# Optimization experiments

Measured on AMD Instinct MI355X. Metric: run time of the kernel, lower is better.

## Reference

```python
import jax, jax.numpy as jnp
import numpy as np

# Constants from the torch module __init__
FACE_INDS = np.array([[0, 1, 2, 3], [0, 4, 2, 6], [0, 1, 4, 5],
                      [1, 3, 5, 7], [2, 3, 6, 7], [4, 5, 6, 7]])  # (6,4)
N_GRID = 11
N_POINTS = N_GRID * N_GRID        # 121
N_FACE = 6
N_KP_HAND = 21
N_CONTACTS = 10
ITA = 0.2
IND1 = np.array([0, 1, 2, 3])
IND2 = np.array([1, 2, 3, 0])


def _bilinear_grid():
    # grid[p, k] = bilinear weights for the 4 face corners, p over 11x11 (u,v)
    g = []
    for u in np.linspace(0.0, 1.0, N_GRID):
        for v in np.linspace(0.0, 1.0, N_GRID):
            g.append([v * (1 - u), v * u, (1 - v) * (1 - u), u * (1 - v)])
    return jnp.asarray(np.array(g, dtype=np.float32))  # (121, 4)


def setup_inputs() -> dict:
    key = jax.random.key(0)
    poses = jax.random.normal(key, (8192, N_KP_HAND + 8, 3), dtype=jnp.float32)
    return {"poses": poses}


def affinity_loss(poses):
    bs = poses.shape[0]
    hand = poses[:, :N_KP_HAND, :]          # (bs, 21, 3)
    obj = poses[:, N_KP_HAND:, :]           # (bs, 8, 3)

    # --- sample_face_points: bilinear sample 121 pts on each of the 6 faces ---
    grid = _bilinear_grid().astype(poses.dtype)        # (121, 4)
    faces = obj[:, FACE_INDS, :]                        # (bs, 6, 4, 3)
    face_points = jnp.einsum('bfkc,pk->bfpc', faces, grid)  # (bs, 6, 121, 3)
    obj_pts = face_points.reshape(bs, N_FACE * N_POINTS, 3)  # (bs, 726, 3)

    xx = jnp.sum(hand * hand, axis=-1)                  # (bs, 21)
    yy = jnp.sum(obj_pts * obj_pts, axis=-1)            # (bs, 726)
    zz = jnp.einsum('bic,bjc->bij', hand, obj_pts)      # (bs, 21, 726)
    pdist = jnp.sqrt(xx[:, :, None] + yy[:, None, :] - 2.0 * zz + 1e-6)
    pdist = pdist.reshape(bs, N_KP_HAND, N_FACE, N_POINTS)

    # --- per (hand kp, face) nearest face point, then global top-10 contacts ---
    dist_h2f = jnp.min(pdist, axis=3)                   # (bs, 21, 6)
    idxs_h2f = jnp.argmin(pdist, axis=3)                # (bs, 21, 6)
    flat = dist_h2f.reshape(bs, N_KP_HAND * N_FACE)     # (bs, 126)
    order = jnp.argsort(flat, axis=1)[:, :N_CONTACTS]   # (bs, 10)
    dist = jnp.take_along_axis(flat, order, axis=1)     # (bs, 10)
    inds_hand = order // N_FACE
    inds_face = order % N_FACE
    b = jnp.arange(bs)[:, None]
    ind_obj = idxs_h2f[b, inds_hand, inds_face]                     # (bs, 10)
    obj_contacts = obj_pts[b, inds_face * N_POINTS + ind_obj]       # (bs, 10, 3)

    # --- get_obj_info: axis endpoints and mean edge length of the bbox ---
    points1 = obj[:, :4, :].mean(axis=1)                # (bs, 3)
    points2 = obj[:, 4:, :].mean(axis=1)                # (bs, 3)
    l1 = jnp.linalg.norm(obj[:, IND1] - obj[:, IND2], axis=-1).mean(1, keepdims=True)
    l2 = jnp.linalg.norm(obj[:, IND1 + 4] - obj[:, IND2 + 4], axis=-1).mean(1, keepdims=True)
    length = (l1 + l2) * 0.5                            # (bs, 1)

    mask1 = (dist < length * ITA).astype(poses.dtype)   # (bs, 10)
    mask = mask1[:, :, None] * mask1[:, None, :]        # (bs, 10, 10)

    direct_vec = points2 - points1                      # (bs, 3)
    dv_norm = jnp.linalg.norm(direct_vec, axis=1, keepdims=True)  # (bs, 1)
    normed_dv = direct_vec / (dv_norm + 1e-5)
    vec_contacts = obj_contacts - points1[:, None, :]   # (bs, 10, 3)
    inner = jnp.sum(direct_vec[:, None, :] * vec_contacts, axis=-1)  # (bs, 10)
    t = inner / (dv_norm + 1e-5)                        # (bs, 10)
    r = points1[:, None, :] + normed_dv[:, None, :] * t[:, :, None]  # (bs, 10, 3)
    normal_vec = obj_contacts - r
    normal_vec = normal_vec / (jnp.linalg.norm(normal_vec, axis=2, keepdims=True) + 1e-5)
    cos_sim = jnp.einsum('bic,bjc->bij', normal_vec, normal_vec)  # (bs, 10, 10)

    return (cos_sim * mask).sum() / (mask.sum() + 1.0)


def reference(poses):
    return affinity_loss(poses)
```

## Files before the change

kernel.cpp:

```cpp
#include <hip/hip_runtime.h>
#include <math.h>

#define NGRID   11
#define NPAIR   126
#define NCONT   10

#define NSUB    64
#define NBUK    128
#define WS_SUB  16
#define WS_BUK  128
#define WS_WORDS (WS_BUK + 2 * NBUK)

#define NBUCKET 256

typedef float v2f __attribute__((ext_vector_type(2)));
#define FMA2(a,b,c) __builtin_elementwise_fma((a),(b),(c))
#define MAX2(a,b)   __builtin_elementwise_max((a),(b))
#define SP2(x)      ((v2f){(x),(x)})

__device__ __constant__ int4 c_face4[6] = {
    {0,1,2,3},{0,4,2,6},{0,1,4,5},{1,3,5,7},{2,3,6,7},{4,5,6,7}};
__device__ __constant__ float c_U[NGRID] = {
    0.0f,0.1f,0.2f,0.3f,0.4f,0.5f,0.6f,0.7f,0.8f,0.9f,1.0f};

__global__ void zero_ws_kernel(float* ws, int n) {
    int t = blockIdx.x * 256 + threadIdx.x;
    if (t < n) ws[t] = 0.0f;
}

__device__ __forceinline__ void pair_coefs(
        const float* __restrict__ obj, float hx, float hy, float hz, int f,
        float& C00, float& C10, float& C01, float& C11,
        float& C20, float& C02, float& C21, float& C12, float& C22) {
    const int4 F = c_face4[f];
    float av[3], bv[3], cv[3], dv[3];
    #pragma unroll
    for (int c = 0; c < 3; ++c) {
        const float P0 = obj[F.x * 3 + c];
        const float P1 = obj[F.y * 3 + c];
        const float P2 = obj[F.z * 3 + c];
        const float P3 = obj[F.w * 3 + c];
        av[c] = P2;
        bv[c] = P3 - P2;
        cv[c] = P0 - P2;
        dv[c] = P1 - P0 - P3 + P2;
    }
    float aa=0.f,bb=0.f,cc=0.f,dd=0.f,ab=0.f,ac=0.f,ad=0.f,bc=0.f,bd=0.f,cd=0.f;
    #pragma unroll
    for (int c = 0; c < 3; ++c) {
        aa += av[c]*av[c]; bb += bv[c]*bv[c];
        cc += cv[c]*cv[c]; dd += dv[c]*dv[c];
        ab += av[c]*bv[c]; ac += av[c]*cv[c];
        ad += av[c]*dv[c]; bc += bv[c]*cv[c];
        bd += bv[c]*dv[c]; cd += cv[c]*dv[c];
    }
    const float hx2 = 2.0f*hx, hy2 = 2.0f*hy, hz2 = 2.0f*hz;
    const float ha2 = fmaf(hx2, av[0], fmaf(hy2, av[1], hz2*av[2]));
    const float hb2 = fmaf(hx2, bv[0], fmaf(hy2, bv[1], hz2*bv[2]));
    const float hc2 = fmaf(hx2, cv[0], fmaf(hy2, cv[1], hz2*cv[2]));
    const float hd2 = fmaf(hx2, dv[0], fmaf(hy2, dv[1], hz2*dv[2]));
    C00 = ha2 - aa;
    C10 = hb2 - 2.f*ab;
    C01 = hc2 - 2.f*ac;
    C11 = hd2 - 2.f*(ad + bc);
    C20 = -bb;  C02 = -cc;  C21 = -2.f*bd;  C12 = -2.f*cd;  C22 = -dd;
}

__device__ __forceinline__ void scan_pair(
        const float* __restrict__ obj, const float* __restrict__ hand,
        int pair, float& d2s, int& ru_out) {
    const int i = pair / 6;
    const int f = pair - i * 6;
    const float hx = hand[i*3+0], hy = hand[i*3+1], hz = hand[i*3+2];
    const float xx = hx*hx + hy*hy + hz*hz;
    float C00,C10,C01,C11,C20,C02,C21,C12,C22;
    pair_coefs(obj, hx, hy, hz, f, C00,C10,C01,C11,C20,C02,C21,C12,C22);

    const float U[NGRID] = {0.0f,0.1f,0.2f,0.3f,0.4f,0.5f,
                            0.6f,0.7f,0.8f,0.9f,1.0f};
    float qb = -3.0e38f;
    int   ru = 0;
    #pragma unroll
    for (int rp = 0; rp < 5; ++rp) {
        const v2f u2 = (v2f){U[2*rp], U[2*rp+1]};
        const v2f A2 = FMA2(FMA2(SP2(C22), u2, SP2(C12)), u2, SP2(C02));
        const v2f A1 = FMA2(FMA2(SP2(C21), u2, SP2(C11)), u2, SP2(C01));
        const v2f A0 = FMA2(FMA2(SP2(C20), u2, SP2(C10)), u2, SP2(C00));
        v2f m2 = A0;
        #pragma unroll
        for (int iv = 1; iv < NGRID; ++iv) {
            const v2f vv = SP2(U[iv]);
            m2 = MAX2(m2, FMA2(FMA2(A2, vv, A1), vv, A0));
        }
        if (m2.x > qb) { qb = m2.x; ru = 2*rp; }
        if (m2.y > qb) { qb = m2.y; ru = 2*rp + 1; }
    }
    {
        const float A2 = fmaf(fmaf(C22,1.f,C12),1.f,C02);
        const float A1 = fmaf(fmaf(C21,1.f,C11),1.f,C01);
        const float A0 = fmaf(fmaf(C20,1.f,C10),1.f,C00);
        float m1 = A0;
        #pragma unroll
        for (int iv = 1; iv < NGRID; ++iv)
            m1 = fmaxf(m1, fmaf(fmaf(A2,U[iv],A1),U[iv],A0));
        if (m1 > qb) { qb = m1; ru = 10; }
    }
    d2s = xx - qb;
    ru_out = ru;
}

__launch_bounds__(256)
__global__ void affinity_kernel(const float* __restrict__ poses,
                                float* __restrict__ ws,
                                float* __restrict__ out,
                                int bs, int nw, int mode) {
    const int lane = threadIdx.x & 63;
    const int wv   = threadIdx.x >> 6;
    const int gw   = blockIdx.x * 4 + wv;
    const bool valid = gw < bs;

    __shared__ float    sh_pose[4][88];
    __shared__ unsigned sh_cand[4][128];
    __shared__ unsigned sh_keys[4][128];
    float*    pose = sh_pose[wv];
    unsigned* cand = sh_cand[wv];
    unsigned* keys = sh_keys[wv];

    if (valid) {
        const float* src = poses + (size_t)gw * 87;
        pose[lane] = src[lane];
        if (lane < 23) pose[64 + lane] = src[64 + lane];
    }
    __threadfence_block();

    float num = 0.f, dnm = 0.f;
    if (valid) {
        const float* hand = pose;
        const float* obj  = pose + 63;

        float l1 = 0.0f, l2 = 0.0f;
        #pragma unroll
        for (int e = 0; e < 4; ++e) {
            const int a = e, b2 = (e + 1) & 3;
            {
                const float dx = obj[a*3+0]-obj[b2*3+0];
                const float dy = obj[a*3+1]-obj[b2*3+1];
                const float dz = obj[a*3+2]-obj[b2*3+2];
                l1 += sqrtf(dx*dx + dy*dy + dz*dz);
            }
            {
                const float dx = obj[(a+4)*3+0]-obj[(b2+4)*3+0];
                const float dy = obj[(a+4)*3+1]-obj[(b2+4)*3+1];
                const float dz = obj[(a+4)*3+2]-obj[(b2+4)*3+2];
                l2 += sqrtf(dx*dx + dy*dy + dz*dz);
            }
        }
        l1 *= 0.25f; l2 *= 0.25f;
        const float L02  = (l1 + l2) * 0.5f * 0.2f;
        const float thrF = L02 * L02 - 1e-6f + 1e-2f;

        float d2A; int ruA;
        scan_pair(obj, hand, lane, d2A, ruA);
        const bool flagA = d2A < thrF;
        const bool hasB  = (lane + 64) < NPAIR;
        float d2B = 3.0e38f; int ruB = 0;
        if (hasB) scan_pair(obj, hand, lane + 64, d2B, ruB);
        const bool flagB = hasB && (d2B < thrF);

        const unsigned long long lt = (1ull << lane) - 1ull;
        const unsigned long long mA = __ballot(flagA);
        const unsigned long long mB = __ballot(flagB);
        const int cntA = __popcll(mA);
        const int cnt  = cntA + __popcll(mB);
        if (flagA) cand[__popcll(mA & lt)] =
            (unsigned)lane | ((unsigned)ruA << 8);
        if (flagB) cand[cntA + __popcll(mB & lt)] =
            (unsigned)(lane + 64) | ((unsigned)ruB << 8);
        __threadfence_block();

        float rkey[2]; float rcx[2], rcy[2], rcz[2]; int rval[2] = {0, 0};
        int n2 = 0;
        #pragma unroll
        for (int c = 0; c < 2; ++c) {
            if (c == 1 && cnt <= 64) break;
            const int idx = c * 64 + lane;
            const bool act = idx < cnt;
            bool pass = false; unsigned key = 0;
            float cx = 0.f, cy = 0.f, cz = 0.f;
            if (act) {
                const unsigned rec = cand[idx];
                const int pair = rec & 0xFF;
                const int ru   = rec >> 8;
                const int i = pair / 6;
                const int f = pair - 6 * i;
                const float hx = hand[i*3+0], hy = hand[i*3+1], hz = hand[i*3+2];
                float C00,C10,C01,C11,C20,C02,C21,C12,C22;
                pair_coefs(obj, hx, hy, hz, f,
                           C00,C10,C01,C11,C20,C02,C21,C12,C22);
                const float u  = c_U[ru];
                const float A2 = fmaf(fmaf(C22,u,C12),u,C02);
                const float A1 = fmaf(fmaf(C21,u,C11),u,C01);
                const float A0 = fmaf(fmaf(C20,u,C10),u,C00);
                const float U[NGRID] = {0.0f,0.1f,0.2f,0.3f,0.4f,0.5f,
                                        0.6f,0.7f,0.8f,0.9f,1.0f};
                float qr = A0; int vb = 0;
                #pragma unroll
                for (int iv = 1; iv < NGRID; ++iv) {
                    const float q = fmaf(fmaf(A2,U[iv],A1),U[iv],A0);
                    if (q > qr) { qr = q; vb = iv; }
                }
                const double du = ru * 0.1;
                const double dv = vb * 0.1;
                const float w0 = (float)(dv * (1.0 - du));
                const float w1 = (float)(dv * du);
                const float w2 = (float)((1.0 - dv) * (1.0 - du));
                const float w3 = (float)(du * (1.0 - dv));
                const int4 F = c_face4[f];
                const int i0 = F.x*3, i1 = F.y*3, i2 = F.z*3, i3 = F.w*3;
                cx = w0*obj[i0+0]+w1*obj[i1+0]+w2*obj[i2+0]+w3*obj[i3+0];
                cy = w0*obj[i0+1]+w1*obj[i1+1]+w2*obj[i2+1]+w3*obj[i3+1];
                cz = w0*obj[i0+2]+w1*obj[i1+2]+w2*obj[i2+2]+w3*obj[i3+2];
                const float xx = hx*hx + hy*hy + hz*hz;
                const float yy = cx*cx + cy*cy + cz*cz;
                const float zz = hx*cx + hy*cy + hz*cz;
                const float d2e = (xx + yy) - 2.0f * zz;
                const float dist = sqrtf(d2e + 1e-6f);
                pass = dist < L02;
                key = (__float_as_uint(fmaxf(d2e, 0.0f)) & 0xFFFFFF80u)
                    | (unsigned)pair;
            }
            const unsigned long long mp = __ballot(pass);
            if (pass) {
                keys[n2 + __popcll(mp & lt)] = key;
                rkey[c] = __uint_as_float(key);
                rcx[c] = cx; rcy[c] = cy; rcz[c] = cz;
                rval[c] = 1;
            }
            n2 += __popcll(mp);
        }
        __threadfence_block();

        const int kwin = n2 < NCONT ? n2 : NCONT;
        float px = 0.f, py = 0.f, pz = 0.f;
        if (rval[0] | rval[1]) {
            const float p1x = (((obj[0] +obj[3]) +obj[6]) +obj[9]) *0.25f;
            const float p1y = (((obj[1] +obj[4]) +obj[7]) +obj[10])*0.25f;
            const float p1z = (((obj[2] +obj[5]) +obj[8]) +obj[11])*0.25f;
            const float p2x = (((obj[12]+obj[15])+obj[18])+obj[21])*0.25f;
            const float p2y = (((obj[13]+obj[16])+obj[19])+obj[22])*0.25f;
            const float p2z = (((obj[14]+obj[17])+obj[20])+obj[23])*0.25f;
            const float dvx = p2x-p1x, dvy = p2y-p1y, dvz = p2z-p1z;
            const float dvn = sqrtf(dvx*dvx + dvy*dvy + dvz*dvz);
            const float den = dvn + 1e-5f;
            const float ndx = dvx/den, ndy = dvy/den, ndz = dvz/den;
            #pragma unroll
            for (int c = 0; c < 2; ++c) {
                if (!rval[c]) continue;
                const unsigned myk = __float_as_uint(rkey[c]);
                int rank = 0;
                for (int j = 0; j < n2; ++j) rank += (keys[j] < myk) ? 1 : 0;
                if (rank < NCONT) {
                    const float cx = rcx[c], cy = rcy[c], cz = rcz[c];
                    const float vcx = cx-p1x, vcy = cy-p1y, vcz = cz-p1z;
                    const float inner = dvx*vcx + dvy*vcy + dvz*vcz;
                    const float tp = inner / den;
                    const float rx = p1x + ndx*tp, ry = p1y + ndy*tp,
                                rz = p1z + ndz*tp;
                    const float nvx = cx-rx, nvy = cy-ry, nvz = cz-rz;
                    const float nvn = sqrtf(nvx*nvx + nvy*nvy + nvz*nvz)
                                    + 1e-5f;
                    px += nvx / nvn; py += nvy / nvn; pz += nvz / nvn;
                }
            }
        }
        #pragma unroll
        for (int off = 32; off >= 1; off >>= 1) {
            px += __shfl_xor(px, off, 64);
            py += __shfl_xor(py, off, 64);
            pz += __shfl_xor(pz, off, 64);
        }
        if (lane == 0) {
            num = px*px + py*py + pz*pz;
            dnm = (float)(kwin * kwin);
        }
    }

    int last = 0;
    if (lane == 0) {
        if (mode) {
            float* bkt = ws + WS_BUK + 2 * (gw & (NBUK - 1));
            const float r0 = atomicAdd(bkt + 0, num);
            const float r1 = atomicAdd(bkt + 1, dnm);
            asm volatile("" :: "v"(r0), "v"(r1) : "memory");
            unsigned* subs = (unsigned*)ws + WS_SUB;
            const unsigned g = (unsigned)gw & (NSUB - 1);
            const unsigned quota = ((unsigned)nw - 1u - g) / NSUB + 1u;
            const unsigned old = atomicAdd(subs + g, 1u);
            if (old + 1u == quota) {
                const unsigned ngroups =
                    (unsigned)nw < NSUB ? (unsigned)nw : NSUB;
                const unsigned m2 = atomicAdd((unsigned*)ws, 1u);
                if (m2 + 1u == ngroups) last = 1;
            }
        } else {
            float* bucket = ws + 2 * (gw & (NBUCKET - 1));
            atomicAdd(bucket + 0, num);
            atomicAdd(bucket + 1, dnm);
        }
    }
    last = __shfl(last, 0, 64);

    if (last) {
        double n = 0.0, d = 0.0;
        for (int k = lane; k < NBUK; k += 64) {
            float* bkt = ws + WS_BUK + 2 * k;
            n += (double)atomicAdd(bkt + 0, 0.0f);
            d += (double)atomicAdd(bkt + 1, 0.0f);
        }
        #pragma unroll
        for (int off = 32; off >= 1; off >>= 1) {
            n += __shfl_xor(n, off, 64);
            d += __shfl_xor(d, off, 64);
        }
        if (lane == 0) out[0] = (float)(n / (d + 1.0));
    }
}

__launch_bounds__(1024)
__global__ void finalize_kernel(const float* __restrict__ ws,
                                float* __restrict__ out, int nslot) {
    const int t = threadIdx.x;
    __shared__ double sh_n[16], sh_d[16];
    double n = 0.0, d = 0.0;
    for (int k = t; k < nslot; k += 1024) {
        n += (double)ws[2 * k + 0];
        d += (double)ws[2 * k + 1];
    }
    #pragma unroll
    for (int off = 32; off >= 1; off >>= 1) {
        n += __shfl_xor(n, off, 64);
        d += __shfl_xor(d, off, 64);
    }
    const int w = t >> 6;
    if ((t & 63) == 0) { sh_n[w] = n; sh_d[w] = d; }
    __syncthreads();
    if (t == 0) {
        double nn = 0.0, dd = 0.0;
        #pragma unroll
        for (int i = 0; i < 16; ++i) { nn += sh_n[i]; dd += sh_d[i]; }
        out[0] = (float)(nn / (dd + 1.0));
    }
}

extern "C" void kernel_launch(void* const* d_in, const int* in_sizes, int n_in,
                              void* d_out, int out_size, void* d_ws, size_t ws_size,
                              hipStream_t stream) {
    const float* poses = (const float*)d_in[0];
    float* out = (float*)d_out;
    float* ws  = (float*)d_ws;
    const int bs = in_sizes[0] / 87;
    const int nblk = (bs + 3) / 4;
    const int nw   = nblk * 4;

    if (ws_size >= (size_t)WS_WORDS * sizeof(float)) {
        hipMemsetAsync(ws, 0, WS_WORDS * sizeof(float), stream);
        hipLaunchKernelGGL(affinity_kernel, dim3(nblk), dim3(256), 0, stream,
                           poses, ws, out, bs, nw, 1);
    } else {
        hipLaunchKernelGGL(zero_ws_kernel, dim3(1), dim3(256), 0, stream,
                           ws, NBUCKET * 2);
        hipLaunchKernelGGL(affinity_kernel, dim3(nblk), dim3(256), 0, stream,
                           poses, ws, out, bs, nw, 0);
        hipLaunchKernelGGL(finalize_kernel, dim3(1), dim3(1024), 0, stream,
                           ws, out, NBUCKET);
    }
}
```

Measured before the change: 90.16 us.

## Split pair scan into separate full-occupancy kernel feeding a select kernel

```diff
diff --git a/kernel.cpp b/kernel.cpp
--- a/kernel.cpp
+++ b/kernel.cpp
@@ -9,7 +9,8 @@
 #define NBUK    128
 #define WS_SUB  16
 #define WS_BUK  128
-#define WS_WORDS (WS_BUK + 2 * NBUK)
+#define WS_HDR  384
+#define WS_REC  1024
 
 #define NBUCKET 256
 
@@ -109,11 +110,95 @@
     ru_out = ru;
 }
 
+__device__ __forceinline__ void exact_contact(
+        const float* __restrict__ obj, const float* __restrict__ hand,
+        int pair, int ru, float& cx, float& cy, float& cz, float& d2e) {
+    const int i = pair / 6;
+    const int f = pair - 6 * i;
+    const float hx = hand[i*3+0], hy = hand[i*3+1], hz = hand[i*3+2];
+    float C00,C10,C01,C11,C20,C02,C21,C12,C22;
+    pair_coefs(obj, hx, hy, hz, f, C00,C10,C01,C11,C20,C02,C21,C12,C22);
+    const float u  = c_U[ru];
+    const float A2 = fmaf(fmaf(C22,u,C12),u,C02);
+    const float A1 = fmaf(fmaf(C21,u,C11),u,C01);
+    const float A0 = fmaf(fmaf(C20,u,C10),u,C00);
+    const float U[NGRID] = {0.0f,0.1f,0.2f,0.3f,0.4f,0.5f,
+                            0.6f,0.7f,0.8f,0.9f,1.0f};
+    float qr = A0; int vb = 0;
+    #pragma unroll
+    for (int iv = 1; iv < NGRID; ++iv) {
+        const float q = fmaf(fmaf(A2,U[iv],A1),U[iv],A0);
+        if (q > qr) { qr = q; vb = iv; }
+    }
+    const double du = ru * 0.1;
+    const double dv = vb * 0.1;
+    const float w0 = (float)(dv * (1.0 - du));
+    const float w1 = (float)(dv * du);
+    const float w2 = (float)((1.0 - dv) * (1.0 - du));
+    const float w3 = (float)(du * (1.0 - dv));
+    const int4 F = c_face4[f];
+    const int i0 = F.x*3, i1 = F.y*3, i2 = F.z*3, i3 = F.w*3;
+    cx = w0*obj[i0+0]+w1*obj[i1+0]+w2*obj[i2+0]+w3*obj[i3+0];
+    cy = w0*obj[i0+1]+w1*obj[i1+1]+w2*obj[i2+1]+w3*obj[i3+1];
+    cz = w0*obj[i0+2]+w1*obj[i1+2]+w2*obj[i2+2]+w3*obj[i3+2];
+    const float xx = hx*hx + hy*hy + hz*hz;
+    const float yy = cx*cx + cy*cy + cz*cz;
+    const float zz = hx*cx + hy*cy + hz*cz;
+    d2e = (xx + yy) - 2.0f * zz;
+}
+
+__device__ __forceinline__ float length_thr(const float* __restrict__ obj) {
+    float l1 = 0.0f, l2 = 0.0f;
+    #pragma unroll
+    for (int e = 0; e < 4; ++e) {
+        const int a = e, b2 = (e + 1) & 3;
+        {
+            const float dx = obj[a*3+0]-obj[b2*3+0];
+            const float dy = obj[a*3+1]-obj[b2*3+1];
+            const float dz = obj[a*3+2]-obj[b2*3+2];
+            l1 += sqrtf(dx*dx + dy*dy + dz*dz);
+        }
+        {
+            const float dx = obj[(a+4)*3+0]-obj[(b2+4)*3+0];
+            const float dy = obj[(a+4)*3+1]-obj[(b2+4)*3+1];
+            const float dz = obj[(a+4)*3+2]-obj[(b2+4)*3+2];
+            l2 += sqrtf(dx*dx + dy*dy + dz*dz);
+        }
+    }
+    l1 *= 0.25f; l2 *= 0.25f;
+    return (l1 + l2) * 0.5f * 0.2f;
+}
+
 __launch_bounds__(256)
-__global__ void affinity_kernel(const float* __restrict__ poses,
-                                float* __restrict__ ws,
-                                float* __restrict__ out,
-                                int bs, int nw, int mode) {
+__global__ void scan_kernel(const float* __restrict__ poses,
+                            float* __restrict__ ws, int bs) {
+    const int t = threadIdx.x;
+    const int half = t >> 7;
+    const int t0 = t & 127;
+    const int batch = blockIdx.x * 2 + half;
+    __shared__ float sh_pose[2][88];
+
+    if (blockIdx.x == 0) {
+        for (int w = t; w < WS_HDR; w += 256) ws[w] = 0.0f;
+    }
+    const bool valid = batch < bs;
+    if (valid && t0 < 87) sh_pose[half][t0] = poses[(size_t)batch * 87 + t0];
+    __syncthreads();
+    if (!valid) return;
+    unsigned rec = __float_as_uint(3.0e38f) & 0xFFFFFFF0u;
+    if (t0 < NPAIR) {
+        float d2s; int ru;
+        scan_pair(sh_pose[half] + 63, sh_pose[half], t0, d2s, ru);
+        rec = (__float_as_uint(d2s) & 0xFFFFFFF0u) | (unsigned)ru;
+    }
+    ((unsigned*)ws)[WS_REC + (size_t)batch * 128 + t0] = rec;
+}
+
+__launch_bounds__(256)
+__global__ void select_kernel(const float* __restrict__ poses,
+                              float* __restrict__ ws,
+                              float* __restrict__ out,
+                              int bs, int nw) {
     const int lane = threadIdx.x & 63;
     const int wv   = threadIdx.x >> 6;
     const int gw   = blockIdx.x * 4 + wv;
@@ -126,46 +211,23 @@
     unsigned* cand = sh_cand[wv];
     unsigned* keys = sh_keys[wv];
 
+    float num = 0.f, dnm = 0.f;
     if (valid) {
         const float* src = poses + (size_t)gw * 87;
         pose[lane] = src[lane];
         if (lane < 23) pose[64 + lane] = src[64 + lane];
-    }
-    __threadfence_block();
-
-    float num = 0.f, dnm = 0.f;
-    if (valid) {
+        const unsigned* recs = (const unsigned*)ws + WS_REC + (size_t)gw * 128;
+        const unsigned recA = recs[lane];
+        const unsigned recB = recs[lane + 64];
+        __threadfence_block();
+
         const float* hand = pose;
         const float* obj  = pose + 63;
-
-        float l1 = 0.0f, l2 = 0.0f;
-        #pragma unroll
-        for (int e = 0; e < 4; ++e) {
-            const int a = e, b2 = (e + 1) & 3;
-            {
-                const float dx = obj[a*3+0]-obj[b2*3+0];
-                const float dy = obj[a*3+1]-obj[b2*3+1];
-                const float dz = obj[a*3+2]-obj[b2*3+2];
-                l1 += sqrtf(dx*dx + dy*dy + dz*dz);
-            }
-            {
-                const float dx = obj[(a+4)*3+0]-obj[(b2+4)*3+0];
-                const float dy = obj[(a+4)*3+1]-obj[(b2+4)*3+1];
-                const float dz = obj[(a+4)*3+2]-obj[(b2+4)*3+2];
-                l2 += sqrtf(dx*dx + dy*dy + dz*dz);
-            }
-        }
-        l1 *= 0.25f; l2 *= 0.25f;
-        const float L02  = (l1 + l2) * 0.5f * 0.2f;
+        const float L02  = length_thr(obj);
         const float thrF = L02 * L02 - 1e-6f + 1e-2f;
 
-        float d2A; int ruA;
-        scan_pair(obj, hand, lane, d2A, ruA);
-        const bool flagA = d2A < thrF;
-        const bool hasB  = (lane + 64) < NPAIR;
-        float d2B = 3.0e38f; int ruB = 0;
-        if (hasB) scan_pair(obj, hand, lane + 64, d2B, ruB);
-        const bool flagB = hasB && (d2B < thrF);
+        const bool flagA = __uint_as_float(recA & 0xFFFFFFF0u) < thrF;
+        const bool flagB = __uint_as_float(recB & 0xFFFFFFF0u) < thrF;
 
         const unsigned long long lt = (1ull << lane) - 1ull;
         const unsigned long long mA = __ballot(flagA);
@@ -173,9 +235,9 @@
         const int cntA = __popcll(mA);
         const int cnt  = cntA + __popcll(mB);
         if (flagA) cand[__popcll(mA & lt)] =
-            (unsigned)lane | ((unsigned)ruA << 8);
+            (unsigned)lane | ((recA & 0xFu) << 8);
         if (flagB) cand[cntA + __popcll(mB & lt)] =
-            (unsigned)(lane + 64) | ((unsigned)ruB << 8);
+            (unsigned)(lane + 64) | ((recB & 0xFu) << 8);
         __threadfence_block();
 
         float rkey[2]; float rcx[2], rcy[2], rcz[2]; int rval[2] = {0, 0};
@@ -188,42 +250,11 @@
             bool pass = false; unsigned key = 0;
             float cx = 0.f, cy = 0.f, cz = 0.f;
             if (act) {
-                const unsigned rec = cand[idx];
-                const int pair = rec & 0xFF;
-                const int ru   = rec >> 8;
-                const int i = pair / 6;
-                const int f = pair - 6 * i;
-                const float hx = hand[i*3+0], hy = hand[i*3+1], hz = hand[i*3+2];
-                float C00,C10,C01,C11,C20,C02,C21,C12,C22;
-                pair_coefs(obj, hx, hy, hz, f,
-                           C00,C10,C01,C11,C20,C02,C21,C12,C22);
-                const float u  = c_U[ru];
-                const float A2 = fmaf(fmaf(C22,u,C12),u,C02);
-                const float A1 = fmaf(fmaf(C21,u,C11),u,C01);
-                const float A0 = fmaf(fmaf(C20,u,C10),u,C00);
-                const float U[NGRID] = {0.0f,0.1f,0.2f,0.3f,0.4f,0.5f,
-                                        0.6f,0.7f,0.8f,0.9f,1.0f};
-                float qr = A0; int vb = 0;
-                #pragma unroll
-                for (int iv = 1; iv < NGRID; ++iv) {
-                    const float q = fmaf(fmaf(A2,U[iv],A1),U[iv],A0);
-                    if (q > qr) { qr = q; vb = iv; }
-                }
-                const double du = ru * 0.1;
-                const double dv = vb * 0.1;
-                const float w0 = (float)(dv * (1.0 - du));
-                const float w1 = (float)(dv * du);
-                const float w2 = (float)((1.0 - dv) * (1.0 - du));
-                const float w3 = (float)(du * (1.0 - dv));
-                const int4 F = c_face4[f];
-                const int i0 = F.x*3, i1 = F.y*3, i2 = F.z*3, i3 = F.w*3;
-                cx = w0*obj[i0+0]+w1*obj[i1+0]+w2*obj[i2+0]+w3*obj[i3+0];
-                cy = w0*obj[i0+1]+w1*obj[i1+1]+w2*obj[i2+1]+w3*obj[i3+1];
-                cz = w0*obj[i0+2]+w1*obj[i1+2]+w2*obj[i2+2]+w3*obj[i3+2];
-                const float xx = hx*hx + hy*hy + hz*hz;
-                const float yy = cx*cx + cy*cy + cz*cz;
-                const float zz = hx*cx + hy*cy + hz*cz;
-                const float d2e = (xx + yy) - 2.0f * zz;
+                const unsigned rc = cand[idx];
+                const int pair = rc & 0xFF;
+                const int ru   = rc >> 8;
+                float d2e;
+                exact_contact(obj, hand, pair, ru, cx, cy, cz, d2e);
                 const float dist = sqrtf(d2e + 1e-6f);
                 pass = dist < L02;
                 key = (__float_as_uint(fmaxf(d2e, 0.0f)) & 0xFFFFFF80u)
@@ -287,25 +318,19 @@
 
     int last = 0;
     if (lane == 0) {
-        if (mode) {
-            float* bkt = ws + WS_BUK + 2 * (gw & (NBUK - 1));
-            const float r0 = atomicAdd(bkt + 0, num);
-            const float r1 = atomicAdd(bkt + 1, dnm);
-            asm volatile("" :: "v"(r0), "v"(r1) : "memory");
-            unsigned* subs = (unsigned*)ws + WS_SUB;
-            const unsigned g = (unsigned)gw & (NSUB - 1);
-            const unsigned quota = ((unsigned)nw - 1u - g) / NSUB + 1u;
-            const unsigned old = atomicAdd(subs + g, 1u);
-            if (old + 1u == quota) {
-                const unsigned ngroups =
-                    (unsigned)nw < NSUB ? (unsigned)nw : NSUB;
-                const unsigned m2 = atomicAdd((unsigned*)ws, 1u);
-                if (m2 + 1u == ngroups) last = 1;
-            }
-        } else {
-            float* bucket = ws + 2 * (gw & (NBUCKET - 1));
-            atomicAdd(bucket + 0, num);
-            atomicAdd(bucket + 1, dnm);
+        float* bkt = ws + WS_BUK + 2 * (gw & (NBUK - 1));
+        const float r0 = atomicAdd(bkt + 0, num);
+        const float r1 = atomicAdd(bkt + 1, dnm);
+        asm volatile("" :: "v"(r0), "v"(r1) : "memory");
+        unsigned* subs = (unsigned*)ws + WS_SUB;
+        const unsigned g = (unsigned)gw & (NSUB - 1);
+        const unsigned quota = ((unsigned)nw - 1u - g) / NSUB + 1u;
+        const unsigned old = atomicAdd(subs + g, 1u);
+        if (old + 1u == quota) {
+            const unsigned ngroups =
+                (unsigned)nw < NSUB ? (unsigned)nw : NSUB;
+            const unsigned m2 = atomicAdd((unsigned*)ws, 1u);
+            if (m2 + 1u == ngroups) last = 1;
         }
     }
     last = __shfl(last, 0, 64);
@@ -323,6 +348,136 @@
             d += __shfl_xor(d, off, 64);
         }
         if (lane == 0) out[0] = (float)(n / (d + 1.0));
+    }
+}
+
+__launch_bounds__(256)
+__global__ void affinity_fallback(const float* __restrict__ poses,
+                                  float* __restrict__ ws, int bs) {
+    const int lane = threadIdx.x & 63;
+    const int wv   = threadIdx.x >> 6;
+    const int gw   = blockIdx.x * 4 + wv;
+    const bool valid = gw < bs;
+
+    __shared__ float    sh_pose[4][88];
+    __shared__ unsigned sh_cand[4][128];
+    __shared__ unsigned sh_keys[4][128];
+    float*    pose = sh_pose[wv];
+    unsigned* cand = sh_cand[wv];
+    unsigned* keys = sh_keys[wv];
+
+    if (valid) {
+        const float* src = poses + (size_t)gw * 87;
+        pose[lane] = src[lane];
+        if (lane < 23) pose[64 + lane] = src[64 + lane];
+    }
+    __threadfence_block();
+
+    float num = 0.f, dnm = 0.f;
+    if (valid) {
+        const float* hand = pose;
+        const float* obj  = pose + 63;
+        const float L02  = length_thr(obj);
+        const float thrF = L02 * L02 - 1e-6f + 1e-2f;
+
+        float d2A; int ruA;
+        scan_pair(obj, hand, lane, d2A, ruA);
+        const bool flagA = d2A < thrF;
+        const bool hasB  = (lane + 64) < NPAIR;
+        float d2B = 3.0e38f; int ruB = 0;
+        if (hasB) scan_pair(obj, hand, lane + 64, d2B, ruB);
+        const bool flagB = hasB && (d2B < thrF);
+
+        const unsigned long long lt = (1ull << lane) - 1ull;
+        const unsigned long long mA = __ballot(flagA);
+        const unsigned long long mB = __ballot(flagB);
+        const int cntA = __popcll(mA);
+        const int cnt  = cntA + __popcll(mB);
+        if (flagA) cand[__popcll(mA & lt)] =
+            (unsigned)lane | ((unsigned)ruA << 8);
+        if (flagB) cand[cntA + __popcll(mB & lt)] =
+            (unsigned)(lane + 64) | ((unsigned)ruB << 8);
+        __threadfence_block();
+
+        float rkey[2]; float rcx[2], rcy[2], rcz[2]; int rval[2] = {0, 0};
+        int n2 = 0;
+        #pragma unroll
+        for (int c = 0; c < 2; ++c) {
+            if (c == 1 && cnt <= 64) break;
+            const int idx = c * 64 + lane;
+            const bool act = idx < cnt;
+            bool pass = false; unsigned key = 0;
+            float cx = 0.f, cy = 0.f, cz = 0.f;
+            if (act) {
+                const unsigned rc = cand[idx];
+                const int pair = rc & 0xFF;
+                const int ru   = rc >> 8;
+                float d2e;
+                exact_contact(obj, hand, pair, ru, cx, cy, cz, d2e);
+                const float dist = sqrtf(d2e + 1e-6f);
+                pass = dist < L02;
+                key = (__float_as_uint(fmaxf(d2e, 0.0f)) & 0xFFFFFF80u)
+                    | (unsigned)pair;
+            }
+            const unsigned long long mp = __ballot(pass);
+            if (pass) {
+                keys[n2 + __popcll(mp & lt)] = key;
+                rkey[c] = __uint_as_float(key);
+                rcx[c] = cx; rcy[c] = cy; rcz[c] = cz;
+                rval[c] = 1;
+            }
+            n2 += __popcll(mp);
+        }
+        __threadfence_block();
+
+        const int kwin = n2 < NCONT ? n2 : NCONT;
+        float px = 0.f, py = 0.f, pz = 0.f;
+        if (rval[0] | rval[1]) {
+            const float p1x = (((obj[0] +obj[3]) +obj[6]) +obj[9]) *0.25f;
+            const float p1y = (((obj[1] +obj[4]) +obj[7]) +obj[10])*0.25f;
+            const float p1z = (((obj[2] +obj[5]) +obj[8]) +obj[11])*0.25f;
+            const float p2x = (((obj[12]+obj[15])+obj[18])+obj[21])*0.25f;
+            const float p2y = (((obj[13]+obj[16])+obj[19])+obj[22])*0.25f;
+            const float p2z = (((obj[14]+obj[17])+obj[20])+obj[23])*0.25f;
+            const float dvx = p2x-p1x, dvy = p2y-p1y, dvz = p2z-p1z;
+            const float dvn = sqrtf(dvx*dvx + dvy*dvy + dvz*dvz);
+            const float den = dvn + 1e-5f;
+            const float ndx = dvx/den, ndy = dvy/den, ndz = dvz/den;
+            #pragma unroll
+            for (int c = 0; c < 2; ++c) {
+                if (!rval[c]) continue;
+                const unsigned myk = __float_as_uint(rkey[c]);
+                int rank = 0;
+                for (int j = 0; j < n2; ++j) rank += (keys[j] < myk) ? 1 : 0;
+                if (rank < NCONT) {
+                    const float cx = rcx[c], cy = rcy[c], cz = rcz[c];
+                    const float vcx = cx-p1x, vcy = cy-p1y, vcz = cz-p1z;
+                    const float inner = dvx*vcx + dvy*vcy + dvz*vcz;
+                    const float tp = inner / den;
+                    const float rx = p1x + ndx*tp, ry = p1y + ndy*tp,
+                                rz = p1z + ndz*tp;
+                    const float nvx = cx-rx, nvy = cy-ry, nvz = cz-rz;
+                    const float nvn = sqrtf(nvx*nvx + nvy*nvy + nvz*nvz)
+                                    + 1e-5f;
+                    px += nvx / nvn; py += nvy / nvn; pz += nvz / nvn;
+                }
+            }
+        }
+        #pragma unroll
+        for (int off = 32; off >= 1; off >>= 1) {
+            px += __shfl_xor(px, off, 64);
+            py += __shfl_xor(py, off, 64);
+            pz += __shfl_xor(pz, off, 64);
+        }
+        if (lane == 0) {
+            num = px*px + py*py + pz*pz;
+            dnm = (float)(kwin * kwin);
+        }
+    }
+    if (lane == 0) {
+        float* bucket = ws + 2 * (gw & (NBUCKET - 1));
+        atomicAdd(bucket + 0, num);
+        atomicAdd(bucket + 1, dnm);
     }
 }
 
@@ -359,18 +514,22 @@
     float* out = (float*)d_out;
     float* ws  = (float*)d_ws;
     const int bs = in_sizes[0] / 87;
-    const int nblk = (bs + 3) / 4;
-    const int nw   = nblk * 4;
-
-    if (ws_size >= (size_t)WS_WORDS * sizeof(float)) {
-        hipMemsetAsync(ws, 0, WS_WORDS * sizeof(float), stream);
-        hipLaunchKernelGGL(affinity_kernel, dim3(nblk), dim3(256), 0, stream,
-                           poses, ws, out, bs, nw, 1);
+
+    const size_t need = ((size_t)WS_REC + (size_t)bs * 128) * sizeof(unsigned);
+    if (ws_size >= need && bs >= 2) {
+        const int nb1 = (bs + 1) / 2;
+        const int nb2 = (bs + 3) / 4;
+        const int nw  = nb2 * 4;
+        hipLaunchKernelGGL(scan_kernel, dim3(nb1), dim3(256), 0, stream,
+                           poses, ws, bs);
+        hipLaunchKernelGGL(select_kernel, dim3(nb2), dim3(256), 0, stream,
+                           poses, ws, out, bs, nw);
     } else {
+        const int nblk = (bs + 3) / 4;
         hipLaunchKernelGGL(zero_ws_kernel, dim3(1), dim3(256), 0, stream,
                            ws, NBUCKET * 2);
-        hipLaunchKernelGGL(affinity_kernel, dim3(nblk), dim3(256), 0, stream,
-                           poses, ws, out, bs, nw, 0);
+        hipLaunchKernelGGL(affinity_fallback, dim3(nblk), dim3(256), 0, stream,
+                           poses, ws, bs);
         hipLaunchKernelGGL(finalize_kernel, dim3(1), dim3(1024), 0, stream,
                            ws, out, NBUCKET);
     }
```

New measurement: 102.0 us. +13.1%, slower.
